# Performance work log

Hardware: AMD Instinct MI355X
Metric: run time of the kernel (lower is better)

Reference implementation:

```python
import jax, jax.numpy as jnp
import numpy as np

N_NODES = 50000
N_EDGES = 1600000
D_IN = 64
D_OUT = 64


def setup_inputs() -> dict:
    key = jax.random.key(0)
    k1, k2, k3, k4 = jax.random.split(key, 4)
    features = jax.random.normal(k1, (N_NODES, D_IN), dtype=jnp.float32)
    edges = jax.random.randint(k2, (2, N_EDGES), 0, N_NODES, dtype=jnp.int64)
    W = jax.random.normal(k3, (D_IN, D_OUT), dtype=jnp.float32) * (1.0 / np.sqrt(D_IN))
    b = jnp.zeros((D_OUT,), dtype=jnp.float32)
    predW = jax.random.normal(k4, (2 * D_OUT, 1), dtype=jnp.float32) * (1.0 / np.sqrt(2 * D_OUT))
    predb = jnp.zeros((1,), dtype=jnp.float32)
    return {"features": features, "edges": edges, "W": W, "b": b, "predW": predW, "predb": predb}


def _gcn_conv(features, edges, W, b):
    # PyG GCNConv: linear transform, add self-loops, symmetric deg^-1/2 norm, sum-aggregate, bias.
    N = features.shape[0]
    x = features @ W  # [N, D_OUT]
    loops = jnp.arange(N, dtype=edges.dtype)
    src = jnp.concatenate([edges[0], loops])  # [E+N]
    dst = jnp.concatenate([edges[1], loops])
    ones = jnp.ones(src.shape[0], dtype=x.dtype)
    deg = jax.ops.segment_sum(ones, dst, num_segments=N)  # includes self-loop
    dinv = jnp.where(deg > 0, jax.lax.rsqrt(deg), 0.0)
    norm = dinv[src] * dinv[dst]  # [E+N]
    msgs = x[src] * norm[:, None]  # gather + scale
    agg = jax.ops.segment_sum(msgs, dst, num_segments=N)  # scatter-add
    return agg + b


def reference(features, edges, W, b, predW, predb):
    h = jax.nn.relu(_gcn_conv(features, edges, W, b))  # [N, D_OUT]
    src, dst = edges[0], edges[1]
    edge_feat = jnp.concatenate([h[src], h[dst]], axis=1)  # [E, 2*D_OUT]
    logits = (edge_feat @ predW + predb).squeeze(-1)  # [E]
    return jax.nn.sigmoid(logits)
```

## Files before the change

kernel.cpp:

```cpp
#include <hip/hip_runtime.h>
#include <cstdint>

#define N_NODES 50000
#define N_EDGES 1600000
#define D 64
#define NPART 8
#define FCAP 22
#define CAP 204800
#define MAXD 256
#define EB4 ((N_EDGES / 4 + 255) / 256)
#define SCH 1024
#define CPB ((N_NODES + SCH - 1) / SCH)

#define NBK 196
#define NBIN 782
#define EPBIN 2048
#define SEGC 36
#define CSRC 8704

typedef __attribute__((ext_vector_type(8))) unsigned short ushort8;
typedef __attribute__((ext_vector_type(4))) int v4i;
typedef __attribute__((ext_vector_type(4))) float v4f;
typedef __attribute__((ext_vector_type(4))) unsigned char v4u8;

__device__ __forceinline__ float bf2f(unsigned short h) {
    union { unsigned u; float f; } x; x.u = ((unsigned)h) << 16; return x.f;
}
__device__ __forceinline__ unsigned short f2bf(float f) {
    union { float f; unsigned u; } x; x.f = f;
    unsigned r = x.u + 0x7FFF + ((x.u >> 16) & 1);
    return (unsigned short)(r >> 16);
}


__global__ __launch_bounds__(256) void k_bin(const int* __restrict__ edges,
                                             unsigned short* __restrict__ seglen,
                                             unsigned* __restrict__ bstore) {
    __shared__ int hist[NBK];
    int tid = threadIdx.x, b = blockIdx.x;
    for (int i = tid; i < NBK; i += 256) hist[i] = 0;
    __syncthreads();
    int e0 = b * EPBIN;
    int kk[8], rk[8];
    unsigned ent[8];
#pragma unroll
    for (int j = 0; j < 8; ++j) {
        int e = e0 + j * 256 + tid;
        kk[j] = -1;
        if (e < N_EDGES) {
            int src = __builtin_nontemporal_load(edges + e);
            int dst = __builtin_nontemporal_load(edges + N_EDGES + e);
            int k = dst >> 8;
            ent[j] = (unsigned)src | ((unsigned)(dst & 255) << 16);
            kk[j] = k;
            rk[j] = atomicAdd(&hist[k], 1);
        }
    }
#pragma unroll
    for (int j = 0; j < 8; ++j) {
        if (kk[j] >= 0 && rk[j] < SEGC)
            bstore[((size_t)kk[j] * NBIN + b) * SEGC + rk[j]] = ent[j];
    }
    __syncthreads();
    for (int i = tid; i < NBK; i += 256)
        seglen[(size_t)b * NBK + i] = (unsigned short)min(hist[i], SEGC);
}

__global__ __launch_bounds__(1024) void k_csr(const unsigned short* __restrict__ seglen,
                                              const unsigned* __restrict__ bstore,
                                              unsigned short* __restrict__ csr,
                                              int* __restrict__ offs,
                                              int* __restrict__ deg,
                                              float* __restrict__ dinv) {
    __shared__ unsigned short slen[NBIN];
    __shared__ int cnt2[256], pfx[256], cur[256];
    int tid = threadIdx.x, k = blockIdx.x;
    if (tid < 256) cnt2[tid] = 0;
    for (int i = tid; i < NBIN; i += 1024) slen[i] = seglen[(size_t)i * NBK + k];
    __syncthreads();
    const unsigned* base = bstore + (size_t)k * NBIN * SEGC;
    const int FT = NBIN * SEGC;
    unsigned ent[28];
#pragma unroll
    for (int j = 0; j < 28; ++j) {
        int f = tid + j * 1024;
        ent[j] = 0xFFFFFFFFu;
        if (f < FT) {
            int s = f / SEGC, i = f - s * SEGC;
            if (i < (int)slen[s])
                ent[j] = base[f];
        }
    }
#pragma unroll
    for (int j = 0; j < 28; ++j)
        if (ent[j] != 0xFFFFFFFFu) atomicAdd(&cnt2[ent[j] >> 16], 1);
    __syncthreads();
    if (tid < 256) pfx[tid] = cnt2[tid];
    __syncthreads();
    for (int off = 1; off < 256; off <<= 1) {
        int t = 0;
        if (tid < 256 && tid >= off) t = pfx[tid - off];
        __syncthreads();
        if (tid < 256) pfx[tid] += t;
        __syncthreads();
    }
    if (tid < 256) cur[tid] = pfx[tid] - cnt2[tid];
    __syncthreads();
#pragma unroll
    for (int j = 0; j < 28; ++j)
        if (ent[j] != 0xFFFFFFFFu) {
            int pos = atomicAdd(&cur[ent[j] >> 16], 1);
            csr[(size_t)k * CSRC + pos] = (unsigned short)(ent[j] & 0xFFFF);
        }
    __syncthreads();
    if (tid < 256) {
        int node = k * 256 + tid;
        if (node < N_NODES) {
            int v0 = cnt2[tid];
            deg[node] = v0;
            offs[node] = k * CSRC + (pfx[tid] - v0);
            dinv[node] = rsqrtf((float)v0 + 1.0f);
        }
        if (k == 0 && tid == 0) dinv[N_NODES] = 0.f;
    }
}

__global__ __launch_bounds__(256) void k_xw2(const float* __restrict__ feat,
                                             const float* __restrict__ W,
                                             unsigned short* __restrict__ xs_bf) {
    __shared__ float Wl[D * D];
    __shared__ float4 ft4[64 * 5];
    int tid = threadIdx.x;
    for (int i = tid; i < D * D; i += 256) Wl[i] = W[i];
    int w = tid >> 6, lane = tid & 63;
    if (blockIdx.x == 0 && tid < 64)
        xs_bf[(size_t)N_NODES * D + tid] = 0;
    int nb = blockIdx.x * 16 + w * 4;
    float4 f;
    f.x = __builtin_nontemporal_load(feat + (size_t)(nb + 0) * D + lane);
    f.y = __builtin_nontemporal_load(feat + (size_t)(nb + 1) * D + lane);
    f.z = __builtin_nontemporal_load(feat + (size_t)(nb + 2) * D + lane);
    f.w = __builtin_nontemporal_load(feat + (size_t)(nb + 3) * D + lane);
    ft4[lane * 5 + w] = f;
    __syncthreads();
    float a0 = 0.f, a1 = 0.f, a2 = 0.f, a3 = 0.f;
#pragma unroll
    for (int k = 0; k < D; ++k) {
        float4 fv = ft4[k * 5 + w];
        float wv = Wl[k * D + lane];
        a0 += fv.x * wv; a1 += fv.y * wv; a2 += fv.z * wv; a3 += fv.w * wv;
    }
    xs_bf[(size_t)(nb + 0) * D + lane] = f2bf(a0);
    xs_bf[(size_t)(nb + 1) * D + lane] = f2bf(a1);
    xs_bf[(size_t)(nb + 2) * D + lane] = f2bf(a2);
    xs_bf[(size_t)(nb + 3) * D + lane] = f2bf(a3);
}

__global__ __launch_bounds__(256) void k_agg3(const unsigned short* __restrict__ xs_bf,
                                              const unsigned short* __restrict__ csr,
                                              const int* __restrict__ offs,
                                              const int* __restrict__ deg,
                                              const float* __restrict__ dinv,
                                              const float* __restrict__ b,
                                              const float* __restrict__ pW,
                                              float* __restrict__ a,
                                              float* __restrict__ c) {
    __shared__ int s_src[4][MAXD];
    int w = threadIdx.x >> 6, lane = threadIdx.x & 63;
    int node = blockIdx.x * 4 + w;
    int cnt = deg[node];
    int off = offs[node];
    for (int i = lane; i < cnt; i += 64)
        s_src[w][i] = (int)csr[(size_t)off + i];
    if (lane == 0) s_src[w][cnt] = node;
    int total = cnt + 1;
    int total8 = (total + 7) & ~7;
    if (lane < total8 - total) s_src[w][total + lane] = N_NODES;
    __syncthreads();

    int g = lane >> 3, q = lane & 7;
    float acc0[8], acc1[8];
#pragma unroll
    for (int j = 0; j < 8; ++j) { acc0[j] = 0.f; acc1[j] = 0.f; }
    for (int i = 0; i < total8; i += 16) {
        int i0 = s_src[w][i + g];
        float dv0 = dinv[i0];
        ushort8 v0 = *(const ushort8*)(xs_bf + (size_t)i0 * D + q * 8);
        if (i + 8 < total8) {
            int i1 = s_src[w][i + 8 + g];
            float dv1 = dinv[i1];
            ushort8 v1 = *(const ushort8*)(xs_bf + (size_t)i1 * D + q * 8);
#pragma unroll
            for (int j = 0; j < 8; ++j) acc1[j] += bf2f(v1[j]) * dv1;
        }
#pragma unroll
        for (int j = 0; j < 8; ++j) acc0[j] += bf2f(v0[j]) * dv0;
    }
    float acc[8];
#pragma unroll
    for (int j = 0; j < 8; ++j) acc[j] = acc0[j] + acc1[j];
#pragma unroll
    for (int off2 = 8; off2 <= 32; off2 <<= 1) {
#pragma unroll
        for (int j = 0; j < 8; ++j) acc[j] += __shfl_xor(acc[j], off2, 64);
    }
    float dn = dinv[node];
    const float4* b4 = (const float4*)b;
    const float4* pW4 = (const float4*)pW;
    float4 b0 = b4[2 * q], b1 = b4[2 * q + 1];
    float4 wa0 = pW4[2 * q], wa1 = pW4[2 * q + 1];
    float4 wc0 = pW4[16 + 2 * q], wc1 = pW4[16 + 2 * q + 1];
    float h0 = fmaxf(acc[0] * dn + b0.x, 0.f);
    float h1 = fmaxf(acc[1] * dn + b0.y, 0.f);
    float h2 = fmaxf(acc[2] * dn + b0.z, 0.f);
    float h3 = fmaxf(acc[3] * dn + b0.w, 0.f);
    float h4 = fmaxf(acc[4] * dn + b1.x, 0.f);
    float h5 = fmaxf(acc[5] * dn + b1.y, 0.f);
    float h6 = fmaxf(acc[6] * dn + b1.z, 0.f);
    float h7 = fmaxf(acc[7] * dn + b1.w, 0.f);
    float p0 = h0 * wa0.x + h1 * wa0.y + h2 * wa0.z + h3 * wa0.w
             + h4 * wa1.x + h5 * wa1.y + h6 * wa1.z + h7 * wa1.w;
    float p1 = h0 * wc0.x + h1 * wc0.y + h2 * wc0.z + h3 * wc0.w
             + h4 * wc1.x + h5 * wc1.y + h6 * wc1.z + h7 * wc1.w;
#pragma unroll
    for (int off2 = 1; off2 <= 4; off2 <<= 1) {
        p0 += __shfl_xor(p0, off2, 64);
        p1 += __shfl_xor(p1, off2, 64);
    }
    if (lane == 0) { a[node] = p0; c[node] = p1; }
}

__global__ __launch_bounds__(256) void k_pred(const int* __restrict__ edges,
                                              const float* __restrict__ a,
                                              const float* __restrict__ c,
                                              const float* __restrict__ pb,
                                              float* __restrict__ out) {
    int t = blockIdx.x * blockDim.x + threadIdx.x;
    if (t >= N_EDGES / 4) return;
    v4i s4 = __builtin_nontemporal_load((const v4i*)edges + t);
    v4i d4 = __builtin_nontemporal_load((const v4i*)(edges + N_EDGES) + t);
    float pbv = pb[0];
    v4f o;
    o[0] = 1.f / (1.f + expf(-(a[s4[0]] + c[d4[0]] + pbv)));
    o[1] = 1.f / (1.f + expf(-(a[s4[1]] + c[d4[1]] + pbv)));
    o[2] = 1.f / (1.f + expf(-(a[s4[2]] + c[d4[2]] + pbv)));
    o[3] = 1.f / (1.f + expf(-(a[s4[3]] + c[d4[3]] + pbv)));
    __builtin_nontemporal_store(o, (v4f*)out + t);
}


__global__ __launch_bounds__(256) void k_xw(const float* __restrict__ feat,
                                            const float* __restrict__ W,
                                            const int* __restrict__ count,
                                            unsigned short* __restrict__ xs_bf) {
    __shared__ float Wl[D * D];
    __shared__ float4 ft4[64 * 5];
    int tid = threadIdx.x;
    for (int i = tid; i < D * D; i += 256) Wl[i] = W[i];
    int w = tid >> 6, lane = tid & 63;
    if (blockIdx.x == 0 && tid < 64)
        xs_bf[(size_t)N_NODES * D + tid] = 0;
    int nb = blockIdx.x * 16 + w * 4;
    float4 f;
    f.x = __builtin_nontemporal_load(feat + (size_t)(nb + 0) * D + lane);
    f.y = __builtin_nontemporal_load(feat + (size_t)(nb + 1) * D + lane);
    f.z = __builtin_nontemporal_load(feat + (size_t)(nb + 2) * D + lane);
    f.w = __builtin_nontemporal_load(feat + (size_t)(nb + 3) * D + lane);
    ft4[lane * 5 + w] = f;
    __syncthreads();
    float a0 = 0.f, a1 = 0.f, a2 = 0.f, a3 = 0.f;
#pragma unroll
    for (int k = 0; k < D; ++k) {
        float4 fv = ft4[k * 5 + w];
        float wv = Wl[k * D + lane];
        a0 += fv.x * wv; a1 += fv.y * wv; a2 += fv.z * wv; a3 += fv.w * wv;
    }
    float dg0 = 1.f, dg1 = 1.f, dg2 = 1.f, dg3 = 1.f;
#pragma unroll
    for (int p = 0; p < NPART; ++p) {
        const int* cp = count + p * N_NODES + nb;
        dg0 += (float)cp[0]; dg1 += (float)cp[1];
        dg2 += (float)cp[2]; dg3 += (float)cp[3];
    }
    xs_bf[(size_t)(nb + 0) * D + lane] = f2bf(a0 * rsqrtf(dg0));
    xs_bf[(size_t)(nb + 1) * D + lane] = f2bf(a1 * rsqrtf(dg1));
    xs_bf[(size_t)(nb + 2) * D + lane] = f2bf(a2 * rsqrtf(dg2));
    xs_bf[(size_t)(nb + 3) * D + lane] = f2bf(a3 * rsqrtf(dg3));
}

__global__ __launch_bounds__(256) void k_hist(const int* __restrict__ edges,
                                              int* __restrict__ count,
                                              unsigned char* __restrict__ rank) {
    int t = blockIdx.x * blockDim.x + threadIdx.x;
    if (t >= N_EDGES / 4) return;
    int p = blockIdx.x & (NPART - 1);
    v4i d4 = __builtin_nontemporal_load((const v4i*)(edges + N_EDGES) + t);
    int* cnt = count + p * N_NODES;
    v4u8 r;
    r[0] = (unsigned char)atomicAdd(&cnt[d4[0]], 1);
    r[1] = (unsigned char)atomicAdd(&cnt[d4[1]], 1);
    r[2] = (unsigned char)atomicAdd(&cnt[d4[2]], 1);
    r[3] = (unsigned char)atomicAdd(&cnt[d4[3]], 1);
    __builtin_nontemporal_store(r, (v4u8*)rank + t);
}

__global__ __launch_bounds__(256) void k_sum(const int4* __restrict__ count4,
                                             int* __restrict__ bsum) {
    int p = blockIdx.x / CPB, j = blockIdx.x - p * CPB;
    int idx4 = j * 256 + threadIdx.x;
    int s = 0;
    if (idx4 < N_NODES / 4) {
        int4 v = count4[p * (N_NODES / 4) + idx4];
        s = v.x + v.y + v.z + v.w;
    }
#pragma unroll
    for (int off = 1; off <= 32; off <<= 1) s += __shfl_xor(s, off, 64);
    __shared__ int red[4];
    int w = threadIdx.x >> 6, lane = threadIdx.x & 63;
    if (lane == 0) red[w] = s;
    __syncthreads();
    if (threadIdx.x == 0)
        bsum[blockIdx.x] = red[0] + red[1] + red[2] + red[3];
}

__global__ __launch_bounds__(512) void k_scanb(const int* __restrict__ bsum,
                                               int* __restrict__ boff,
                                               int* __restrict__ start_t) {
    int w = threadIdx.x >> 6, lane = threadIdx.x & 63;
    int v = (lane < CPB) ? bsum[w * CPB + lane] : 0;
    int incl = v;
#pragma unroll
    for (int off = 1; off < 64; off <<= 1) {
        int t = __shfl_up(incl, off, 64);
        if (lane >= off) incl += t;
    }
    if (lane < CPB) boff[w * CPB + lane] = incl - v;
    if (lane == CPB - 1) start_t[N_NODES * NPART + w] = incl;
}

__global__ __launch_bounds__(256) void k_scat(const int4* __restrict__ count4,
                                              const int* __restrict__ boff,
                                              int* __restrict__ start_t) {
    int p = blockIdx.x / CPB, j = blockIdx.x - p * CPB;
    int idx4 = j * 256 + threadIdx.x;
    bool valid = idx4 < N_NODES / 4;
    int4 v = {0, 0, 0, 0};
    int s = 0;
    if (valid) {
        v = count4[p * (N_NODES / 4) + idx4];
        s = v.x + v.y + v.z + v.w;
    }
    int w = threadIdx.x >> 6, lane = threadIdx.x & 63;
    int incl = s;
#pragma unroll
    for (int off = 1; off < 64; off <<= 1) {
        int t = __shfl_up(incl, off, 64);
        if (lane >= off) incl += t;
    }
    __shared__ int wsum[4];
    if (lane == 63) wsum[w] = incl;
    __syncthreads();
    int wbase = 0;
    for (int k = 0; k < w; ++k) wbase += wsum[k];
    int excl = wbase + incl - s;
    if (valid) {
        int base = boff[p * CPB + j] + excl;
        int n = idx4 * 4;
        start_t[(n + 0) * NPART + p] = base;
        start_t[(n + 1) * NPART + p] = base + v.x;
        start_t[(n + 2) * NPART + p] = base + v.x + v.y;
        start_t[(n + 3) * NPART + p] = base + v.x + v.y + v.z;
    }
}

__global__ __launch_bounds__(256) void k_place(const int* __restrict__ edges,
                                               const int* __restrict__ start_t,
                                               const unsigned char* __restrict__ rank,
                                               unsigned short* __restrict__ sorted) {
    int t = blockIdx.x * blockDim.x + threadIdx.x;
    if (t >= N_EDGES / 4) return;
    int p = blockIdx.x & (NPART - 1);
    v4i s4 = __builtin_nontemporal_load((const v4i*)edges + t);
    v4i d4 = __builtin_nontemporal_load((const v4i*)(edges + N_EDGES) + t);
    v4u8 r4 = __builtin_nontemporal_load((const v4u8*)rank + t);
    unsigned short* srt = sorted + p * CAP;
    srt[start_t[d4[0] * NPART + p] + r4[0]] = (unsigned short)s4[0];
    srt[start_t[d4[1] * NPART + p] + r4[1]] = (unsigned short)s4[1];
    srt[start_t[d4[2] * NPART + p] + r4[2]] = (unsigned short)s4[2];
    srt[start_t[d4[3] * NPART + p] + r4[3]] = (unsigned short)s4[3];
}

__global__ __launch_bounds__(256) void k_agg(const unsigned short* __restrict__ xs_bf,
                                             const int* __restrict__ start_t,
                                             const unsigned short* __restrict__ sorted,
                                             const float* __restrict__ b,
                                             const float* __restrict__ pW,
                                             float* __restrict__ a,
                                             float* __restrict__ c) {
    __shared__ int s_src[4][MAXD];
    int w = threadIdx.x >> 6, lane = threadIdx.x & 63;
    int node = blockIdx.x * 4 + w;
    int total = 0, total_pad = 0;
    if (node < N_NODES) {
        const int4* st4 = (const int4*)(start_t + node * NPART);
        int4 lo0 = st4[0], lo1 = st4[1], hi0 = st4[2], hi1 = st4[3];
        int sa[8] = {lo0.x, lo0.y, lo0.z, lo0.w, lo1.x, lo1.y, lo1.z, lo1.w};
        int ea[8] = {hi0.x, hi0.y, hi0.z, hi0.w, hi1.x, hi1.y, hi1.z, hi1.w};
#pragma unroll
        for (int p = 0; p < NPART; ++p) {
            int s0 = sa[p], cnt = ea[p] - s0;
            if (total + cnt > MAXD - 17) cnt = MAXD - 17 - total;
            int base = p * CAP + s0;
            for (int i = lane; i < cnt; i += 64)
                s_src[w][total + i] = (int)__builtin_nontemporal_load(sorted + base + i);
            total += cnt;
        }
        if (lane == 0) s_src[w][total] = node;
        total += 1;
        total_pad = (total + 15) & ~15;
        if (lane < total_pad - total) s_src[w][total + lane] = N_NODES;
    }
    __syncthreads();
    if (node >= N_NODES) return;
    int g = lane >> 3, q = lane & 7;
    float acc0[8], acc1[8];
#pragma unroll
    for (int j = 0; j < 8; ++j) { acc0[j] = 0.f; acc1[j] = 0.f; }
    for (int i = 0; i < total_pad; i += 16) {
        int i0 = s_src[w][i + g];
        int i1 = s_src[w][i + 8 + g];
        ushort8 v0 = *(const ushort8*)(xs_bf + (size_t)i0 * D + q * 8);
        ushort8 v1 = *(const ushort8*)(xs_bf + (size_t)i1 * D + q * 8);
#pragma unroll
        for (int j = 0; j < 8; ++j) acc0[j] += bf2f(v0[j]);
#pragma unroll
        for (int j = 0; j < 8; ++j) acc1[j] += bf2f(v1[j]);
    }
    float acc[8];
#pragma unroll
    for (int j = 0; j < 8; ++j) acc[j] = acc0[j] + acc1[j];
#pragma unroll
    for (int off = 8; off <= 32; off <<= 1) {
#pragma unroll
        for (int j = 0; j < 8; ++j) acc[j] += __shfl_xor(acc[j], off, 64);
    }
    float dinv = rsqrtf((float)total);
    const float4* b4 = (const float4*)b;
    const float4* pW4 = (const float4*)pW;
    float4 b0 = b4[2 * q], b1 = b4[2 * q + 1];
    float4 wa0 = pW4[2 * q], wa1 = pW4[2 * q + 1];
    float4 wc0 = pW4[16 + 2 * q], wc1 = pW4[16 + 2 * q + 1];
    float h0 = fmaxf(acc[0] * dinv + b0.x, 0.f);
    float h1 = fmaxf(acc[1] * dinv + b0.y, 0.f);
    float h2 = fmaxf(acc[2] * dinv + b0.z, 0.f);
    float h3 = fmaxf(acc[3] * dinv + b0.w, 0.f);
    float h4 = fmaxf(acc[4] * dinv + b1.x, 0.f);
    float h5 = fmaxf(acc[5] * dinv + b1.y, 0.f);
    float h6 = fmaxf(acc[6] * dinv + b1.z, 0.f);
    float h7 = fmaxf(acc[7] * dinv + b1.w, 0.f);
    float p0 = h0 * wa0.x + h1 * wa0.y + h2 * wa0.z + h3 * wa0.w
             + h4 * wa1.x + h5 * wa1.y + h6 * wa1.z + h7 * wa1.w;
    float p1 = h0 * wc0.x + h1 * wc0.y + h2 * wc0.z + h3 * wc0.w
             + h4 * wc1.x + h5 * wc1.y + h6 * wc1.z + h7 * wc1.w;
#pragma unroll
    for (int off = 1; off <= 4; off <<= 1) {
        p0 += __shfl_xor(p0, off, 64);
        p1 += __shfl_xor(p1, off, 64);
    }
    if (lane == 0) { a[node] = p0; c[node] = p1; }
}


extern "C" void kernel_launch(void* const* d_in, const int* in_sizes, int n_in,
                              void* d_out, int out_size, void* d_ws, size_t ws_size,
                              hipStream_t stream) {
    const float* feat  = (const float*)d_in[0];
    const int*   edges = (const int*)d_in[1];
    const float* W     = (const float*)d_in[2];
    const float* b     = (const float*)d_in[3];
    const float* predW = (const float*)d_in[4];
    const float* predb = (const float*)d_in[5];
    float* out = (float*)d_out;
    char* ws = (char*)d_ws;

    const size_t FUSED_NEED = 26789760;

    if (ws_size >= FUSED_NEED) {
        unsigned short* csr    = (unsigned short*)(ws + 0);
        int*            offs   = (int*)(ws + 3411968);
        int*            deg    = (int*)(ws + 3611968);
        float*          dinv   = (float*)(ws + 3811968);
        float*          a      = (float*)(ws + 4011984);
        float*          c      = (float*)(ws + 4211984);
        unsigned short* seglen = (unsigned short*)(ws + 4411984);
        unsigned*       bstore = (unsigned*)(ws + 4718592);
        unsigned short* xs_bf  = (unsigned short*)(ws + 4718592);

        k_bin <<<NBIN, 256, 0, stream>>>(edges, seglen, bstore);
        k_csr <<<NBK, 1024, 0, stream>>>(seglen, bstore, csr, offs, deg, dinv);
        k_xw2 <<<N_NODES / 16, 256, 0, stream>>>(feat, W, xs_bf);
        k_agg3<<<N_NODES / 4, 256, 0, stream>>>(xs_bf, csr, offs, deg, dinv, b, predW, a, c);
        k_pred<<<EB4, 256, 0, stream>>>(edges, a, c, predb, out);
    } else {
        int*            count   = (int*)(ws + 0);
        int*            start_t = (int*)(ws + 1600000);
        int*            bsum    = (int*)(ws + 3200048);
        int*            boff    = (int*)(ws + 3201616);
        float*          a       = (float*)(ws + 3210000);
        float*          c       = (float*)(ws + 3410000);
        unsigned char*  rank    = (unsigned char*)(ws + 3610000);
        unsigned short* sorted  = (unsigned short*)(ws + 5210000);
        unsigned short* xs_bf   = (unsigned short*)(ws + 8486800);

        hipMemsetAsync(count, 0, NPART * N_NODES * sizeof(int), stream);
        k_hist <<<EB4, 256, 0, stream>>>(edges, count, rank);
        k_sum  <<<NPART * CPB, 256, 0, stream>>>((const int4*)count, bsum);
        k_scanb<<<1, 512, 0, stream>>>(bsum, boff, start_t);
        k_scat <<<NPART * CPB, 256, 0, stream>>>((const int4*)count, boff, start_t);
        k_xw   <<<N_NODES / 16, 256, 0, stream>>>(feat, W, count, xs_bf);
        k_place<<<EB4, 256, 0, stream>>>(edges, start_t, rank, sorted);
        k_agg  <<<(N_NODES + 3) / 4, 256, 0, stream>>>(xs_bf, start_t, sorted, b, predW, a, c);
        k_pred <<<EB4, 256, 0, stream>>>(edges, a, c, predb, out);
    }
}
```

Baseline: 101.6 us.

## Fuse edge binning and feature transform into one heterogeneous launch

Edge binning and the X·W transform now run in a single kernel, with every fifth block doing binning and the rest doing the matmul. xs_bf moves to its own workspace region after bstore so the two phases no longer alias. This removes one kernel launch and lets the memory-bound binning overlap with the compute-bound transform. The cost is a larger workspace requirement, a fallback path when the workspace is too small, and a union of shared-memory allocations in every block that may reduce occupancy.

New measurement: 97.85 us, median of 2. 3.7% less time.

```diff
diff --git a/kernel.cpp b/kernel.cpp
--- a/kernel.cpp
+++ b/kernel.cpp
@@ -17,6 +17,7 @@
 #define EPBIN 2048
 #define SEGC 36
 #define CSRC 8704
+#define XWB (N_NODES / 16)
 
 typedef __attribute__((ext_vector_type(8))) unsigned short ushort8;
 typedef __attribute__((ext_vector_type(4))) int v4i;
@@ -33,11 +34,41 @@
 }
 
 
-__global__ __launch_bounds__(256) void k_bin(const int* __restrict__ edges,
-                                             unsigned short* __restrict__ seglen,
-                                             unsigned* __restrict__ bstore) {
-    __shared__ int hist[NBK];
-    int tid = threadIdx.x, b = blockIdx.x;
+__device__ __forceinline__ void xw_body(int xb, int tid,
+                                        const float* __restrict__ feat,
+                                        const float* __restrict__ W,
+                                        unsigned short* __restrict__ xs_bf,
+                                        float* Wl, float4* ft4) {
+    for (int i = tid; i < D * D; i += 256) Wl[i] = W[i];
+    int w = tid >> 6, lane = tid & 63;
+    if (xb == 0 && tid < 64)
+        xs_bf[(size_t)N_NODES * D + tid] = 0;
+    int nb = xb * 16 + w * 4;
+    float4 f;
+    f.x = __builtin_nontemporal_load(feat + (size_t)(nb + 0) * D + lane);
+    f.y = __builtin_nontemporal_load(feat + (size_t)(nb + 1) * D + lane);
+    f.z = __builtin_nontemporal_load(feat + (size_t)(nb + 2) * D + lane);
+    f.w = __builtin_nontemporal_load(feat + (size_t)(nb + 3) * D + lane);
+    ft4[lane * 5 + w] = f;
+    __syncthreads();
+    float a0 = 0.f, a1 = 0.f, a2 = 0.f, a3 = 0.f;
+#pragma unroll
+    for (int k = 0; k < D; ++k) {
+        float4 fv = ft4[k * 5 + w];
+        float wv = Wl[k * D + lane];
+        a0 += fv.x * wv; a1 += fv.y * wv; a2 += fv.z * wv; a3 += fv.w * wv;
+    }
+    xs_bf[(size_t)(nb + 0) * D + lane] = f2bf(a0);
+    xs_bf[(size_t)(nb + 1) * D + lane] = f2bf(a1);
+    xs_bf[(size_t)(nb + 2) * D + lane] = f2bf(a2);
+    xs_bf[(size_t)(nb + 3) * D + lane] = f2bf(a3);
+}
+
+__device__ __forceinline__ void bin_body(int b, int tid,
+                                         const int* __restrict__ edges,
+                                         unsigned short* __restrict__ seglen,
+                                         unsigned* __restrict__ bstore,
+                                         int* hist) {
     for (int i = tid; i < NBK; i += 256) hist[i] = 0;
     __syncthreads();
     int e0 = b * EPBIN;
@@ -64,6 +95,40 @@
     __syncthreads();
     for (int i = tid; i < NBK; i += 256)
         seglen[(size_t)b * NBK + i] = (unsigned short)min(hist[i], SEGC);
+}
+
+
+__global__ __launch_bounds__(256) void k_binxw(const int* __restrict__ edges,
+                                               unsigned short* __restrict__ seglen,
+                                               unsigned* __restrict__ bstore,
+                                               const float* __restrict__ feat,
+                                               const float* __restrict__ W,
+                                               unsigned short* __restrict__ xs_bf) {
+    __shared__ float Wl[D * D];
+    __shared__ float4 ft4[64 * 5];
+    __shared__ int hist[NBK];
+    int tid = threadIdx.x, bid = blockIdx.x;
+    if (bid % 5 == 0) {
+        bin_body(bid / 5, tid, edges, seglen, bstore, hist);
+    } else {
+        int xb = bid - bid / 5 - 1;
+        xw_body(xb, tid, feat, W, xs_bf, Wl, ft4);
+    }
+}
+
+__global__ __launch_bounds__(256) void k_bin(const int* __restrict__ edges,
+                                             unsigned short* __restrict__ seglen,
+                                             unsigned* __restrict__ bstore) {
+    __shared__ int hist[NBK];
+    bin_body(blockIdx.x, threadIdx.x, edges, seglen, bstore, hist);
+}
+
+__global__ __launch_bounds__(256) void k_xw2(const float* __restrict__ feat,
+                                             const float* __restrict__ W,
+                                             unsigned short* __restrict__ xs_bf) {
+    __shared__ float Wl[D * D];
+    __shared__ float4 ft4[64 * 5];
+    xw_body(blockIdx.x, threadIdx.x, feat, W, xs_bf, Wl, ft4);
 }
 
 __global__ __launch_bounds__(1024) void k_csr(const unsigned short* __restrict__ seglen,
@@ -123,37 +188,6 @@
         }
         if (k == 0 && tid == 0) dinv[N_NODES] = 0.f;
     }
-}
-
-__global__ __launch_bounds__(256) void k_xw2(const float* __restrict__ feat,
-                                             const float* __restrict__ W,
-                                             unsigned short* __restrict__ xs_bf) {
-    __shared__ float Wl[D * D];
-    __shared__ float4 ft4[64 * 5];
-    int tid = threadIdx.x;
-    for (int i = tid; i < D * D; i += 256) Wl[i] = W[i];
-    int w = tid >> 6, lane = tid & 63;
-    if (blockIdx.x == 0 && tid < 64)
-        xs_bf[(size_t)N_NODES * D + tid] = 0;
-    int nb = blockIdx.x * 16 + w * 4;
-    float4 f;
-    f.x = __builtin_nontemporal_load(feat + (size_t)(nb + 0) * D + lane);
-    f.y = __builtin_nontemporal_load(feat + (size_t)(nb + 1) * D + lane);
-    f.z = __builtin_nontemporal_load(feat + (size_t)(nb + 2) * D + lane);
-    f.w = __builtin_nontemporal_load(feat + (size_t)(nb + 3) * D + lane);
-    ft4[lane * 5 + w] = f;
-    __syncthreads();
-    float a0 = 0.f, a1 = 0.f, a2 = 0.f, a3 = 0.f;
-#pragma unroll
-    for (int k = 0; k < D; ++k) {
-        float4 fv = ft4[k * 5 + w];
-        float wv = Wl[k * D + lane];
-        a0 += fv.x * wv; a1 += fv.y * wv; a2 += fv.z * wv; a3 += fv.w * wv;
-    }
-    xs_bf[(size_t)(nb + 0) * D + lane] = f2bf(a0);
-    xs_bf[(size_t)(nb + 1) * D + lane] = f2bf(a1);
-    xs_bf[(size_t)(nb + 2) * D + lane] = f2bf(a2);
-    xs_bf[(size_t)(nb + 3) * D + lane] = f2bf(a3);
 }
 
 __global__ __launch_bounds__(256) void k_agg3(const unsigned short* __restrict__ xs_bf,
@@ -483,24 +517,41 @@
     float* out = (float*)d_out;
     char* ws = (char*)d_ws;
 
-    const size_t FUSED_NEED = 26789760;
-
-    if (ws_size >= FUSED_NEED) {
+    const size_t OFF_OFFS   = 3411968;
+    const size_t OFF_DEG    = 3611968;
+    const size_t OFF_DINV   = 3811968;
+    const size_t OFF_A      = 4011984;
+    const size_t OFF_C      = 4211984;
+    const size_t OFF_SEGLEN = 4411984;
+    const size_t OFF_BSTORE = 4718592;
+    const size_t BSTORE_SZ  = (size_t)NBK * NBIN * SEGC * 4;
+    const size_t NEED_B = OFF_BSTORE + BSTORE_SZ;
+    const size_t NEED_A = NEED_B + 6400128;
+
+    if (ws_size >= NEED_B) {
         unsigned short* csr    = (unsigned short*)(ws + 0);
-        int*            offs   = (int*)(ws + 3411968);
-        int*            deg    = (int*)(ws + 3611968);
-        float*          dinv   = (float*)(ws + 3811968);
-        float*          a      = (float*)(ws + 4011984);
-        float*          c      = (float*)(ws + 4211984);
-        unsigned short* seglen = (unsigned short*)(ws + 4411984);
-        unsigned*       bstore = (unsigned*)(ws + 4718592);
-        unsigned short* xs_bf  = (unsigned short*)(ws + 4718592);
-
-        k_bin <<<NBIN, 256, 0, stream>>>(edges, seglen, bstore);
-        k_csr <<<NBK, 1024, 0, stream>>>(seglen, bstore, csr, offs, deg, dinv);
-        k_xw2 <<<N_NODES / 16, 256, 0, stream>>>(feat, W, xs_bf);
-        k_agg3<<<N_NODES / 4, 256, 0, stream>>>(xs_bf, csr, offs, deg, dinv, b, predW, a, c);
-        k_pred<<<EB4, 256, 0, stream>>>(edges, a, c, predb, out);
+        int*            offs   = (int*)(ws + OFF_OFFS);
+        int*            deg    = (int*)(ws + OFF_DEG);
+        float*          dinv   = (float*)(ws + OFF_DINV);
+        float*          a      = (float*)(ws + OFF_A);
+        float*          c      = (float*)(ws + OFF_C);
+        unsigned short* seglen = (unsigned short*)(ws + OFF_SEGLEN);
+        unsigned*       bstore = (unsigned*)(ws + OFF_BSTORE);
+
+        if (ws_size >= NEED_A) {
+            unsigned short* xs_bf = (unsigned short*)(ws + NEED_B);
+            k_binxw<<<NBIN + XWB, 256, 0, stream>>>(edges, seglen, bstore, feat, W, xs_bf);
+            k_csr  <<<NBK, 1024, 0, stream>>>(seglen, bstore, csr, offs, deg, dinv);
+            k_agg3 <<<N_NODES / 4, 256, 0, stream>>>(xs_bf, csr, offs, deg, dinv, b, predW, a, c);
+            k_pred <<<EB4, 256, 0, stream>>>(edges, a, c, predb, out);
+        } else {
+            unsigned short* xs_bf = (unsigned short*)(ws + OFF_BSTORE);
+            k_bin <<<NBIN, 256, 0, stream>>>(edges, seglen, bstore);
+            k_csr <<<NBK, 1024, 0, stream>>>(seglen, bstore, csr, offs, deg, dinv);
+            k_xw2 <<<N_NODES / 16, 256, 0, stream>>>(feat, W, xs_bf);
+            k_agg3<<<N_NODES / 4, 256, 0, stream>>>(xs_bf, csr, offs, deg, dinv, b, predW, a, c);
+            k_pred<<<EB4, 256, 0, stream>>>(edges, a, c, predb, out);
+        }
     } else {
         int*            count   = (int*)(ws + 0);
         int*            start_t = (int*)(ws + 1600000);
```
